# Kernel tuning notes

Hardware: AMD Instinct MI355X
Metric: run time of the kernel (lower is better)

Reference implementation:

```python
import jax, jax.numpy as jnp
import numpy as np
from jax import lax

E, C, H, W = 256, 128, 56, 56          # edges, stage-2 channels, spatial
NC, NP, NL, LL, FEAT = 200, 512, 64, 8, 64  # corners, corner-edge pairs, loops, loop len, loop feat
EDGE_DIM = 2 * C                        # 256 (image pooled + coord)
LOOP_IN = EDGE_DIM + 2                  # 258 (LoopEncoder input channels)


def _conv1d_relu(x, w, b):
    # x: [N, Cin, L]; ReflectionPad1d(1) + Conv1d(k=3) + ReLU
    x = jnp.pad(x, ((0, 0), (0, 0), (1, 1)), mode='reflect')
    y = lax.conv_general_dilated(x, w, (1,), 'VALID', dimension_numbers=('NCH', 'OIH', 'NCH'))
    return jax.nn.relu(y + b[None, :, None])


def setup_inputs() -> dict:
    key = jax.random.key(0)
    ks = jax.random.split(key, 16)
    p = lambda i, shape: jax.random.normal(ks[i], shape, jnp.float32) * 0.05
    return {
        'image_x': jax.random.normal(ks[0], (E, C, H, W), jnp.float32),
        'coord_x': jax.random.normal(ks[1], (E, C, 1, 1), jnp.float32),
        'corners': jax.random.uniform(ks[2], (NC, 2), jnp.float32),
        'corner_edge_pairs': jnp.stack([jax.random.randint(ks[3], (NP,), 0, NC),
                                        jax.random.randint(ks[4], (NP,), 0, E)], axis=1),
        'edge_corner': jax.random.randint(ks[5], (E, 2), 0, NC),
        'loops': jax.random.randint(ks[6], (NL, LL), 0, NC),
        'W_ep1': p(7, (64, EDGE_DIM)), 'b_ep1': jnp.zeros((64,), jnp.float32),
        'W_ep2': p(8, (1, 64)), 'b_ep2': jnp.zeros((1,), jnp.float32),
        'Wc0': p(9, (64, LOOP_IN, 3)), 'bc0': jnp.zeros((64,), jnp.float32),
        'Wc1': p(10, (64, 64, 3)), 'bc1': jnp.zeros((64,), jnp.float32),
        'Wc2': p(11, (64, 64, 3)), 'bc2': jnp.zeros((64,), jnp.float32),
        'Wl1': p(12, (32, 64)), 'bl1': jnp.zeros((32,), jnp.float32),
        'Wl2': p(13, (1, 32)), 'bl2': jnp.zeros((1,), jnp.float32),
        'W_agg': p(14, (C, C + FEAT)),
    }


def reference(image_x, coord_x, corners, corner_edge_pairs, edge_corner, loops,
              W_ep1, b_ep1, W_ep2, b_ep2, Wc0, bc0, Wc1, bc1, Wc2, bc2,
              Wl1, bl1, Wl2, bl2, W_agg):
    # edge features: global max-pool of per-edge image features + coord features
    edge_x = jnp.concatenate([image_x.max(axis=(-2, -1)), coord_x[:, :, 0, 0]], axis=1)  # [E, 2C]
    edge_conf = jax.nn.sigmoid(jax.nn.relu(edge_x @ W_ep1.T + b_ep1) @ W_ep2.T + b_ep2).ravel()  # [E]

    # scatter-mean edge features onto corners (index_add_ in torch)
    cf = jax.ops.segment_sum(edge_x[corner_edge_pairs[:, 1]], corner_edge_pairs[:, 0], num_segments=NC)
    cnt = jax.ops.segment_sum(jnp.ones((NP,), jnp.float32), corner_edge_pairs[:, 0], num_segments=NC)
    corner_features = cf / jnp.maximum(cnt, 1.0)[:, None]  # [NC, 2C]

    # LoopEncoder over each loop's corner sequence (vectorized over loops)
    loop_inp = jnp.concatenate([corner_features[loops], corners[loops]], axis=-1)  # [NL, LL, 2C+2]
    h = loop_inp.transpose(0, 2, 1)  # [NL, 2C+2, LL]
    h = _conv1d_relu(h, Wc0, bc0)
    h = _conv1d_relu(h, Wc1, bc1)
    h = _conv1d_relu(h, Wc2, bc2)
    loop_features = h.max(-1)  # [NL, 64]
    loop_conf = jax.nn.sigmoid(jax.nn.relu(loop_features @ Wl1.T + bl1) @ Wl2.T + bl2).ravel()  # [NL]

    # loop-edge incidence: edge (a,b) is in loop iff (a,b) appears as consecutive pair (either order)
    prev = jnp.roll(loops, 1, axis=1)
    nxt = jnp.roll(loops, -1, axis=1)
    pairs = jnp.concatenate([jnp.stack([loops, prev], -1), jnp.stack([loops, nxt], -1)], axis=1)  # [NL, 2LL, 2]
    loop_edges = (edge_corner[None, :, None, :] == pairs[:, None, :, :]).all(-1).any(-1)
    loop_edges = loop_edges.astype(jnp.float32)  # [NL, E]

    # confidence-weighted average of loop features per edge
    wgt = loop_conf[:, None, None] * loop_edges[..., None]  # [NL, E, 1]
    coord_features = (loop_features[:, None, :] * wgt).sum(0) / jnp.maximum(wgt.sum(0), 1e-4)  # [E, 64]

    # coord_aggregate: 1x1 conv (no bias) + ReLU
    out = jax.nn.relu(jnp.concatenate([coord_x[:, :, 0, 0], coord_features], axis=1) @ W_agg.T)  # [E, C]
    return out, edge_conf, loop_conf, loop_edges
```

## Files before the change

### kernel.cpp

```cpp
#include <hip/hip_runtime.h>
#include <math.h>

#define E_      256
#define C_      128
#define S_      3136
#define NC_     200
#define NP_     512
#define NL_     64
#define LL_     8
#define EDGE_DIM_ 256
#define LOOP_IN_  258
#define FEAT_   64

__global__ __launch_bounds__(256) void pool_kernel(const float* __restrict__ image_x,
                                                   float* __restrict__ edge_x) {
    int row  = blockIdx.x * 4 + (threadIdx.x >> 6);
    int lane = threadIdx.x & 63;
    const float4* p = reinterpret_cast<const float4*>(image_x) + (size_t)row * (S_ / 4);

    float m = -INFINITY;
    #pragma unroll
    for (int it = 0; it < 12; ++it) {
        float4 v = p[lane + it * 64];
        m = fmaxf(m, fmaxf(fmaxf(v.x, v.y), fmaxf(v.z, v.w)));
    }
    if (lane < 16) {
        float4 v = p[768 + lane];
        m = fmaxf(m, fmaxf(fmaxf(v.x, v.y), fmaxf(v.z, v.w)));
    }
    #pragma unroll
    for (int off = 32; off; off >>= 1) m = fmaxf(m, __shfl_down(m, off));
    if (lane == 0) {
        int e = row >> 7, c = row & 127;
        edge_x[e * EDGE_DIM_ + c] = m;
    }
}

__global__ void coord_copy_kernel(const float* __restrict__ coord_x,
                                  float* __restrict__ edge_x) {
    int i = blockIdx.x * 256 + threadIdx.x;
    int e = i >> 7, c = i & 127;
    edge_x[e * EDGE_DIM_ + C_ + c] = coord_x[i];
}

__global__ __launch_bounds__(64) void edge_conf_kernel(const float* __restrict__ edge_x,
                                                       const float* __restrict__ W1,
                                                       const float* __restrict__ b1,
                                                       const float* __restrict__ W2,
                                                       const float* __restrict__ b2,
                                                       float* __restrict__ out_conf) {
    int e = blockIdx.x, j = threadIdx.x;
    const float* x = edge_x + e * EDGE_DIM_;
    float acc = b1[j];
    for (int i = 0; i < EDGE_DIM_; ++i) acc += x[i] * W1[j * EDGE_DIM_ + i];
    float h = fmaxf(acc, 0.f) * W2[j];
    #pragma unroll
    for (int off = 32; off; off >>= 1) h += __shfl_down(h, off);
    if (j == 0) out_conf[e] = 1.f / (1.f + __expf(-(h + b2[0])));
}

__global__ __launch_bounds__(256) void corner_kernel(const float* __restrict__ edge_x,
                                                     const int* __restrict__ pairs,
                                                     float* __restrict__ corner_features) {
    __shared__ int sp[NP_ * 2];
    int corner = blockIdx.x;
    for (int i = threadIdx.x; i < NP_ * 2; i += 256) sp[i] = pairs[i];
    __syncthreads();
    int c = threadIdx.x;
    float sum = 0.f, cnt = 0.f;
    for (int p = 0; p < NP_; ++p) {
        if (sp[p * 2] == corner) { sum += edge_x[sp[p * 2 + 1] * EDGE_DIM_ + c]; cnt += 1.f; }
    }
    corner_features[corner * EDGE_DIM_ + c] = sum / fmaxf(cnt, 1.f);
}

__global__ __launch_bounds__(64) void loop_enc_kernel(
        const float* __restrict__ corner_features, const float* __restrict__ corners,
        const int* __restrict__ loops,
        const float* __restrict__ Wc0, const float* __restrict__ bc0,
        const float* __restrict__ Wc1, const float* __restrict__ bc1,
        const float* __restrict__ Wc2, const float* __restrict__ bc2,
        const float* __restrict__ Wl1, const float* __restrict__ bl1,
        const float* __restrict__ Wl2, const float* __restrict__ bl2,
        float* __restrict__ loop_features, float* __restrict__ out_loop_conf) {
    __shared__ float inp[LOOP_IN_][LL_];
    __shared__ float ha[64][LL_];
    __shared__ float hb[64][LL_];
    __shared__ float lf[64];
    __shared__ int cidx[LL_];

    int l = blockIdx.x, tid = threadIdx.x;
    if (tid < LL_) cidx[tid] = loops[l * LL_ + tid];
    __syncthreads();
    for (int idx = tid; idx < LOOP_IN_ * LL_; idx += 64) {
        int i = idx / LL_, j = idx % LL_;
        float v = (i < EDGE_DIM_) ? corner_features[cidx[j] * EDGE_DIM_ + i]
                                  : corners[cidx[j] * 2 + (i - EDGE_DIM_)];
        inp[i][j] = v;
    }
    __syncthreads();

    const int rm1[8] = {1, 0, 1, 2, 3, 4, 5, 6};
    const int rp1[8] = {1, 2, 3, 4, 5, 6, 7, 6};
    int o = tid;

    {
        float acc[LL_];
        float b = bc0[o];
        #pragma unroll
        for (int t = 0; t < LL_; ++t) acc[t] = b;
        for (int i = 0; i < LOOP_IN_; ++i) {
            float w0 = Wc0[(o * LOOP_IN_ + i) * 3 + 0];
            float w1 = Wc0[(o * LOOP_IN_ + i) * 3 + 1];
            float w2 = Wc0[(o * LOOP_IN_ + i) * 3 + 2];
            #pragma unroll
            for (int t = 0; t < LL_; ++t)
                acc[t] += w0 * inp[i][rm1[t]] + w1 * inp[i][t] + w2 * inp[i][rp1[t]];
        }
        #pragma unroll
        for (int t = 0; t < LL_; ++t) ha[o][t] = fmaxf(acc[t], 0.f);
    }
    __syncthreads();

    {
        float acc[LL_];
        float b = bc1[o];
        #pragma unroll
        for (int t = 0; t < LL_; ++t) acc[t] = b;
        for (int i = 0; i < 64; ++i) {
            float w0 = Wc1[(o * 64 + i) * 3 + 0];
            float w1 = Wc1[(o * 64 + i) * 3 + 1];
            float w2 = Wc1[(o * 64 + i) * 3 + 2];
            #pragma unroll
            for (int t = 0; t < LL_; ++t)
                acc[t] += w0 * ha[i][rm1[t]] + w1 * ha[i][t] + w2 * ha[i][rp1[t]];
        }
        #pragma unroll
        for (int t = 0; t < LL_; ++t) hb[o][t] = fmaxf(acc[t], 0.f);
    }
    __syncthreads();

    {
        float acc[LL_];
        float b = bc2[o];
        #pragma unroll
        for (int t = 0; t < LL_; ++t) acc[t] = b;
        for (int i = 0; i < 64; ++i) {
            float w0 = Wc2[(o * 64 + i) * 3 + 0];
            float w1 = Wc2[(o * 64 + i) * 3 + 1];
            float w2 = Wc2[(o * 64 + i) * 3 + 2];
            #pragma unroll
            for (int t = 0; t < LL_; ++t)
                acc[t] += w0 * hb[i][rm1[t]] + w1 * hb[i][t] + w2 * hb[i][rp1[t]];
        }
        float m = -INFINITY;
        #pragma unroll
        for (int t = 0; t < LL_; ++t) m = fmaxf(m, fmaxf(acc[t], 0.f));
        lf[o] = m;
        loop_features[l * FEAT_ + o] = m;
    }
    __syncthreads();

    float part = 0.f;
    if (tid < 32) {
        float a = bl1[tid];
        for (int o2 = 0; o2 < 64; ++o2) a += lf[o2] * Wl1[tid * 64 + o2];
        part = fmaxf(a, 0.f) * Wl2[tid];
    }
    #pragma unroll
    for (int off = 32; off; off >>= 1) part += __shfl_down(part, off);
    if (tid == 0) out_loop_conf[l] = 1.f / (1.f + __expf(-(part + bl2[0])));
}

__global__ __launch_bounds__(256) void loop_edges_kernel(const int* __restrict__ loops,
                                                         const int* __restrict__ edge_corner,
                                                         float* __restrict__ out_le) {
    __shared__ int lp[LL_];
    int l = blockIdx.x;
    if (threadIdx.x < LL_) lp[threadIdx.x] = loops[l * LL_ + threadIdx.x];
    __syncthreads();
    int e = threadIdx.x;
    int a = edge_corner[e * 2], b = edge_corner[e * 2 + 1];
    bool hit = false;
    #pragma unroll
    for (int j = 0; j < LL_; ++j) {
        int x = lp[j], pv = lp[(j + LL_ - 1) & 7], nx = lp[(j + 1) & 7];
        hit = hit || (a == x && (b == pv || b == nx));
    }
    out_le[l * E_ + e] = hit ? 1.f : 0.f;
}

__global__ __launch_bounds__(128) void final_kernel(const float* __restrict__ coord_x,
                                                    const float* __restrict__ loop_features,
                                                    const float* __restrict__ loop_conf,
                                                    const float* __restrict__ loop_edges,
                                                    const float* __restrict__ W_agg,
                                                    float* __restrict__ out) {
    __shared__ float cf[FEAT_];
    int e = blockIdx.x, tid = threadIdx.x;
    if (tid < FEAT_) {
        float num = 0.f, den = 0.f;
        for (int l = 0; l < NL_; ++l) {
            float w = loop_conf[l] * loop_edges[l * E_ + e];
            den += w;
            num += w * loop_features[l * FEAT_ + tid];
        }
        cf[tid] = num / fmaxf(den, 1e-4f);
    }
    __syncthreads();
    int c = tid;
    const float* wr = W_agg + c * (C_ + FEAT_);
    float acc = 0.f;
    for (int j = 0; j < C_; ++j) acc += coord_x[e * C_ + j] * wr[j];
    for (int f = 0; f < FEAT_; ++f) acc += cf[f] * wr[C_ + f];
    out[e * C_ + c] = fmaxf(acc, 0.f);
}

extern "C" void kernel_launch(void* const* d_in, const int* in_sizes, int n_in,
                              void* d_out, int out_size, void* d_ws, size_t ws_size,
                              hipStream_t stream) {
    const float* image_x     = (const float*)d_in[0];
    const float* coord_x     = (const float*)d_in[1];
    const float* corners     = (const float*)d_in[2];
    const int*   cep         = (const int*)d_in[3];
    const int*   edge_corner = (const int*)d_in[4];
    const int*   loops       = (const int*)d_in[5];
    const float* W_ep1 = (const float*)d_in[6];
    const float* b_ep1 = (const float*)d_in[7];
    const float* W_ep2 = (const float*)d_in[8];
    const float* b_ep2 = (const float*)d_in[9];
    const float* Wc0   = (const float*)d_in[10];
    const float* bc0   = (const float*)d_in[11];
    const float* Wc1   = (const float*)d_in[12];
    const float* bc1   = (const float*)d_in[13];
    const float* Wc2   = (const float*)d_in[14];
    const float* bc2   = (const float*)d_in[15];
    const float* Wl1   = (const float*)d_in[16];
    const float* bl1   = (const float*)d_in[17];
    const float* Wl2   = (const float*)d_in[18];
    const float* bl2   = (const float*)d_in[19];
    const float* W_agg = (const float*)d_in[20];

    float* out       = (float*)d_out;
    float* out_main  = out;
    float* out_econf = out + E_ * C_;
    float* out_lconf = out_econf + E_;
    float* out_le    = out_lconf + NL_;

    float* edge_x          = (float*)d_ws;
    float* corner_features = edge_x + E_ * EDGE_DIM_;
    float* loop_features   = corner_features + NC_ * EDGE_DIM_;

    pool_kernel<<<dim3(E_ * C_ / 4), dim3(256), 0, stream>>>(image_x, edge_x);
    coord_copy_kernel<<<dim3(E_ * C_ / 256), dim3(256), 0, stream>>>(coord_x, edge_x);
    edge_conf_kernel<<<dim3(E_), dim3(64), 0, stream>>>(edge_x, W_ep1, b_ep1, W_ep2, b_ep2, out_econf);
    corner_kernel<<<dim3(NC_), dim3(256), 0, stream>>>(edge_x, cep, corner_features);
    loop_enc_kernel<<<dim3(NL_), dim3(64), 0, stream>>>(corner_features, corners, loops,
                                                        Wc0, bc0, Wc1, bc1, Wc2, bc2,
                                                        Wl1, bl1, Wl2, bl2,
                                                        loop_features, out_lconf);
    loop_edges_kernel<<<dim3(NL_), dim3(256), 0, stream>>>(loops, edge_corner, out_le);
    final_kernel<<<dim3(E_), dim3(128), 0, stream>>>(coord_x, loop_features, out_lconf,
                                                     out_le, W_agg, out_main);
}
```

Measured before the change: 685.9 us.

## Fuse small kernels and split loop-encoder convolutions across four waves

Moves the coord copy into the pool kernel, and merges edge-confidence, corner averaging and loop-edge incidence into one kernel that branches on block index. This removes several launches and the gaps between them. The loop encoder now uses 256 threads, with each wave handling a quarter of the input channels and the partial sums reduced through shared memory. That adds parallelism to a 64-block kernel at the cost of extra syncs and shared-memory traffic. The pool kernel dominates runtime (about 411 MB read), so the gain is limited to launch overhead and the latency of the small serial stages.

```diff
diff --git a/kernel.cpp b/kernel.cpp
--- a/kernel.cpp
+++ b/kernel.cpp
@@ -13,6 +13,7 @@
 #define FEAT_   64
 
 __global__ __launch_bounds__(256) void pool_kernel(const float* __restrict__ image_x,
+                                                   const float* __restrict__ coord_x,
                                                    float* __restrict__ edge_x) {
     int row  = blockIdx.x * 4 + (threadIdx.x >> 6);
     int lane = threadIdx.x & 63;
@@ -33,48 +34,73 @@
     if (lane == 0) {
         int e = row >> 7, c = row & 127;
         edge_x[e * EDGE_DIM_ + c] = m;
-    }
-}
-
-__global__ void coord_copy_kernel(const float* __restrict__ coord_x,
-                                  float* __restrict__ edge_x) {
-    int i = blockIdx.x * 256 + threadIdx.x;
-    int e = i >> 7, c = i & 127;
-    edge_x[e * EDGE_DIM_ + C_ + c] = coord_x[i];
-}
-
-__global__ __launch_bounds__(64) void edge_conf_kernel(const float* __restrict__ edge_x,
-                                                       const float* __restrict__ W1,
-                                                       const float* __restrict__ b1,
-                                                       const float* __restrict__ W2,
-                                                       const float* __restrict__ b2,
-                                                       float* __restrict__ out_conf) {
-    int e = blockIdx.x, j = threadIdx.x;
-    const float* x = edge_x + e * EDGE_DIM_;
-    float acc = b1[j];
-    for (int i = 0; i < EDGE_DIM_; ++i) acc += x[i] * W1[j * EDGE_DIM_ + i];
-    float h = fmaxf(acc, 0.f) * W2[j];
-    #pragma unroll
-    for (int off = 32; off; off >>= 1) h += __shfl_down(h, off);
-    if (j == 0) out_conf[e] = 1.f / (1.f + __expf(-(h + b2[0])));
-}
-
-__global__ __launch_bounds__(256) void corner_kernel(const float* __restrict__ edge_x,
-                                                     const int* __restrict__ pairs,
-                                                     float* __restrict__ corner_features) {
-    __shared__ int sp[NP_ * 2];
-    int corner = blockIdx.x;
-    for (int i = threadIdx.x; i < NP_ * 2; i += 256) sp[i] = pairs[i];
-    __syncthreads();
-    int c = threadIdx.x;
-    float sum = 0.f, cnt = 0.f;
-    for (int p = 0; p < NP_; ++p) {
-        if (sp[p * 2] == corner) { sum += edge_x[sp[p * 2 + 1] * EDGE_DIM_ + c]; cnt += 1.f; }
-    }
-    corner_features[corner * EDGE_DIM_ + c] = sum / fmaxf(cnt, 1.f);
-}
-
-__global__ __launch_bounds__(64) void loop_enc_kernel(
+        edge_x[e * EDGE_DIM_ + C_ + c] = coord_x[row];
+    }
+}
+
+#define MID_A_  64
+#define MID_B_  (MID_A_ + NC_)
+#define MID_N_  (MID_B_ + NL_)
+
+__global__ __launch_bounds__(256) void mid_kernel(const float* __restrict__ edge_x,
+                                                  const float* __restrict__ W1,
+                                                  const float* __restrict__ b1,
+                                                  const float* __restrict__ W2,
+                                                  const float* __restrict__ b2,
+                                                  const int* __restrict__ pairs,
+                                                  const int* __restrict__ loops,
+                                                  const int* __restrict__ edge_corner,
+                                                  float* __restrict__ out_econf,
+                                                  float* __restrict__ corner_features,
+                                                  float* __restrict__ out_le) {
+    __shared__ float smem[4 * EDGE_DIM_];
+    int b = blockIdx.x, tid = threadIdx.x;
+
+    if (b < MID_A_) {
+        float* xs = smem;
+        for (int idx = tid; idx < 4 * EDGE_DIM_; idx += 256)
+            xs[idx] = edge_x[b * 4 * EDGE_DIM_ + idx];
+        __syncthreads();
+        int w = tid >> 6, j = tid & 63;
+        int e = b * 4 + w;
+        const float* x = xs + w * EDGE_DIM_;
+        const float* wr = W1 + j * EDGE_DIM_;
+        float acc = b1[j];
+        #pragma unroll 8
+        for (int i = 0; i < EDGE_DIM_; ++i) acc += x[i] * wr[i];
+        float h = fmaxf(acc, 0.f) * W2[j];
+        #pragma unroll
+        for (int off = 32; off; off >>= 1) h += __shfl_down(h, off);
+        if (j == 0) out_econf[e] = 1.f / (1.f + __expf(-(h + b2[0])));
+    } else if (b < MID_B_) {
+        int* sp = reinterpret_cast<int*>(smem);
+        int corner = b - MID_A_;
+        for (int i = tid; i < NP_ * 2; i += 256) sp[i] = pairs[i];
+        __syncthreads();
+        int c = tid;
+        float sum = 0.f, cnt = 0.f;
+        for (int p = 0; p < NP_; ++p) {
+            if (sp[p * 2] == corner) { sum += edge_x[sp[p * 2 + 1] * EDGE_DIM_ + c]; cnt += 1.f; }
+        }
+        corner_features[corner * EDGE_DIM_ + c] = sum / fmaxf(cnt, 1.f);
+    } else {
+        int* lp = reinterpret_cast<int*>(smem);
+        int l = b - MID_B_;
+        if (tid < LL_) lp[tid] = loops[l * LL_ + tid];
+        __syncthreads();
+        int e = tid;
+        int a = edge_corner[e * 2], bb = edge_corner[e * 2 + 1];
+        bool hit = false;
+        #pragma unroll
+        for (int j = 0; j < LL_; ++j) {
+            int x = lp[j], pv = lp[(j + LL_ - 1) & 7], nx = lp[(j + 1) & 7];
+            hit = hit || (a == x && (bb == pv || bb == nx));
+        }
+        out_le[l * E_ + e] = hit ? 1.f : 0.f;
+    }
+}
+
+__global__ __launch_bounds__(256) void loop_enc_kernel(
         const float* __restrict__ corner_features, const float* __restrict__ corners,
         const int* __restrict__ loops,
         const float* __restrict__ Wc0, const float* __restrict__ bc0,
@@ -83,111 +109,125 @@
         const float* __restrict__ Wl1, const float* __restrict__ bl1,
         const float* __restrict__ Wl2, const float* __restrict__ bl2,
         float* __restrict__ loop_features, float* __restrict__ out_loop_conf) {
-    __shared__ float inp[LOOP_IN_][LL_];
-    __shared__ float ha[64][LL_];
-    __shared__ float hb[64][LL_];
+    __shared__ float inp[LOOP_IN_ * LL_];
+    __shared__ float part[4 * 64 * 9];
+    __shared__ float ha[64 * 9];
+    __shared__ float hb[64 * 9];
     __shared__ float lf[64];
     __shared__ int cidx[LL_];
 
     int l = blockIdx.x, tid = threadIdx.x;
+    int o = tid & 63, s = tid >> 6;
     if (tid < LL_) cidx[tid] = loops[l * LL_ + tid];
     __syncthreads();
-    for (int idx = tid; idx < LOOP_IN_ * LL_; idx += 64) {
-        int i = idx / LL_, j = idx % LL_;
-        float v = (i < EDGE_DIM_) ? corner_features[cidx[j] * EDGE_DIM_ + i]
-                                  : corners[cidx[j] * 2 + (i - EDGE_DIM_)];
-        inp[i][j] = v;
+    for (int idx = tid; idx < LOOP_IN_ * LL_; idx += 256) {
+        int i = idx >> 3, j = idx & 7;
+        inp[idx] = (i < EDGE_DIM_) ? corner_features[cidx[j] * EDGE_DIM_ + i]
+                                   : corners[cidx[j] * 2 + (i - EDGE_DIM_)];
     }
     __syncthreads();
 
     const int rm1[8] = {1, 0, 1, 2, 3, 4, 5, 6};
     const int rp1[8] = {1, 2, 3, 4, 5, 6, 7, 6};
-    int o = tid;
 
     {
         float acc[LL_];
-        float b = bc0[o];
-        #pragma unroll
-        for (int t = 0; t < LL_; ++t) acc[t] = b;
-        for (int i = 0; i < LOOP_IN_; ++i) {
+        #pragma unroll
+        for (int t = 0; t < LL_; ++t) acc[t] = 0.f;
+        int lo = s * 64 + (s < 2 ? s : 2);
+        int hi = lo + (s < 2 ? 65 : 64);
+        for (int i = lo; i < hi; ++i) {
             float w0 = Wc0[(o * LOOP_IN_ + i) * 3 + 0];
             float w1 = Wc0[(o * LOOP_IN_ + i) * 3 + 1];
             float w2 = Wc0[(o * LOOP_IN_ + i) * 3 + 2];
+            const float* ip = inp + i * LL_;
             #pragma unroll
             for (int t = 0; t < LL_; ++t)
-                acc[t] += w0 * inp[i][rm1[t]] + w1 * inp[i][t] + w2 * inp[i][rp1[t]];
-        }
-        #pragma unroll
-        for (int t = 0; t < LL_; ++t) ha[o][t] = fmaxf(acc[t], 0.f);
+                acc[t] += w0 * ip[rm1[t]] + w1 * ip[t] + w2 * ip[rp1[t]];
+        }
+        #pragma unroll
+        for (int t = 0; t < LL_; ++t) part[(s * 64 + o) * 9 + t] = acc[t];
+    }
+    __syncthreads();
+    if (tid < 64) {
+        #pragma unroll
+        for (int t = 0; t < LL_; ++t) {
+            float v = bc0[tid];
+            #pragma unroll
+            for (int ss = 0; ss < 4; ++ss) v += part[(ss * 64 + tid) * 9 + t];
+            ha[tid * 9 + t] = fmaxf(v, 0.f);
+        }
     }
     __syncthreads();
 
     {
         float acc[LL_];
-        float b = bc1[o];
-        #pragma unroll
-        for (int t = 0; t < LL_; ++t) acc[t] = b;
-        for (int i = 0; i < 64; ++i) {
+        #pragma unroll
+        for (int t = 0; t < LL_; ++t) acc[t] = 0.f;
+        for (int i = s * 16; i < s * 16 + 16; ++i) {
             float w0 = Wc1[(o * 64 + i) * 3 + 0];
             float w1 = Wc1[(o * 64 + i) * 3 + 1];
             float w2 = Wc1[(o * 64 + i) * 3 + 2];
+            const float* ip = ha + i * 9;
             #pragma unroll
             for (int t = 0; t < LL_; ++t)
-                acc[t] += w0 * ha[i][rm1[t]] + w1 * ha[i][t] + w2 * ha[i][rp1[t]];
-        }
-        #pragma unroll
-        for (int t = 0; t < LL_; ++t) hb[o][t] = fmaxf(acc[t], 0.f);
+                acc[t] += w0 * ip[rm1[t]] + w1 * ip[t] + w2 * ip[rp1[t]];
+        }
+        #pragma unroll
+        for (int t = 0; t < LL_; ++t) part[(s * 64 + o) * 9 + t] = acc[t];
+    }
+    __syncthreads();
+    if (tid < 64) {
+        #pragma unroll
+        for (int t = 0; t < LL_; ++t) {
+            float v = bc1[tid];
+            #pragma unroll
+            for (int ss = 0; ss < 4; ++ss) v += part[(ss * 64 + tid) * 9 + t];
+            hb[tid * 9 + t] = fmaxf(v, 0.f);
+        }
     }
     __syncthreads();
 
     {
         float acc[LL_];
-        float b = bc2[o];
-        #pragma unroll
-        for (int t = 0; t < LL_; ++t) acc[t] = b;
-        for (int i = 0; i < 64; ++i) {
+        #pragma unroll
+        for (int t = 0; t < LL_; ++t) acc[t] = 0.f;
+        for (int i = s * 16; i < s * 16 + 16; ++i) {
             float w0 = Wc2[(o * 64 + i) * 3 + 0];
             float w1 = Wc2[(o * 64 + i) * 3 + 1];
             float w2 = Wc2[(o * 64 + i) * 3 + 2];
+            const float* ip = hb + i * 9;
             #pragma unroll
             for (int t = 0; t < LL_; ++t)
-                acc[t] += w0 * hb[i][rm1[t]] + w1 * hb[i][t] + w2 * hb[i][rp1[t]];
-        }
+                acc[t] += w0 * ip[rm1[t]] + w1 * ip[t] + w2 * ip[rp1[t]];
+        }
+        #pragma unroll
+        for (int t = 0; t < LL_; ++t) part[(s * 64 + o) * 9 + t] = acc[t];
+    }
+    __syncthreads();
+    if (tid < 64) {
         float m = -INFINITY;
         #pragma unroll
-        for (int t = 0; t < LL_; ++t) m = fmaxf(m, fmaxf(acc[t], 0.f));
-        lf[o] = m;
-        loop_features[l * FEAT_ + o] = m;
-    }
-    __syncthreads();
-
-    float part = 0.f;
+        for (int t = 0; t < LL_; ++t) {
+            float v = bc2[tid];
+            #pragma unroll
+            for (int ss = 0; ss < 4; ++ss) v += part[(ss * 64 + tid) * 9 + t];
+            m = fmaxf(m, fmaxf(v, 0.f));
+        }
+        lf[tid] = m;
+        loop_features[l * FEAT_ + tid] = m;
+    }
+    __syncthreads();
+
+    float pv = 0.f;
     if (tid < 32) {
         float a = bl1[tid];
         for (int o2 = 0; o2 < 64; ++o2) a += lf[o2] * Wl1[tid * 64 + o2];
-        part = fmaxf(a, 0.f) * Wl2[tid];
+        pv = fmaxf(a, 0.f) * Wl2[tid];
     }
     #pragma unroll
-    for (int off = 32; off; off >>= 1) part += __shfl_down(part, off);
-    if (tid == 0) out_loop_conf[l] = 1.f / (1.f + __expf(-(part + bl2[0])));
-}
-
-__global__ __launch_bounds__(256) void loop_edges_kernel(const int* __restrict__ loops,
-                                                         const int* __restrict__ edge_corner,
-                                                         float* __restrict__ out_le) {
-    __shared__ int lp[LL_];
-    int l = blockIdx.x;
-    if (threadIdx.x < LL_) lp[threadIdx.x] = loops[l * LL_ + threadIdx.x];
-    __syncthreads();
-    int e = threadIdx.x;
-    int a = edge_corner[e * 2], b = edge_corner[e * 2 + 1];
-    bool hit = false;
-    #pragma unroll
-    for (int j = 0; j < LL_; ++j) {
-        int x = lp[j], pv = lp[(j + LL_ - 1) & 7], nx = lp[(j + 1) & 7];
-        hit = hit || (a == x && (b == pv || b == nx));
-    }
-    out_le[l * E_ + e] = hit ? 1.f : 0.f;
+    for (int off = 32; off; off >>= 1) pv += __shfl_down(pv, off);
+    if (tid == 0) out_loop_conf[l] = 1.f / (1.f + __expf(-(pv + bl2[0])));
 }
 
 __global__ __launch_bounds__(128) void final_kernel(const float* __restrict__ coord_x,
@@ -251,15 +291,14 @@
     float* corner_features = edge_x + E_ * EDGE_DIM_;
     float* loop_features   = corner_features + NC_ * EDGE_DIM_;
 
-    pool_kernel<<<dim3(E_ * C_ / 4), dim3(256), 0, stream>>>(image_x, edge_x);
-    coord_copy_kernel<<<dim3(E_ * C_ / 256), dim3(256), 0, stream>>>(coord_x, edge_x);
-    edge_conf_kernel<<<dim3(E_), dim3(64), 0, stream>>>(edge_x, W_ep1, b_ep1, W_ep2, b_ep2, out_econf);
-    corner_kernel<<<dim3(NC_), dim3(256), 0, stream>>>(edge_x, cep, corner_features);
-    loop_enc_kernel<<<dim3(NL_), dim3(64), 0, stream>>>(corner_features, corners, loops,
-                                                        Wc0, bc0, Wc1, bc1, Wc2, bc2,
-                                                        Wl1, bl1, Wl2, bl2,
-                                                        loop_features, out_lconf);
-    loop_edges_kernel<<<dim3(NL_), dim3(256), 0, stream>>>(loops, edge_corner, out_le);
+    pool_kernel<<<dim3(E_ * C_ / 4), dim3(256), 0, stream>>>(image_x, coord_x, edge_x);
+    mid_kernel<<<dim3(MID_N_), dim3(256), 0, stream>>>(edge_x, W_ep1, b_ep1, W_ep2, b_ep2,
+                                                       cep, loops, edge_corner,
+                                                       out_econf, corner_features, out_le);
+    loop_enc_kernel<<<dim3(NL_), dim3(256), 0, stream>>>(corner_features, corners, loops,
+                                                         Wc0, bc0, Wc1, bc1, Wc2, bc2,
+                                                         Wl1, bl1, Wl2, bl2,
+                                                         loop_features, out_lconf);
     final_kernel<<<dim3(E_), dim3(128), 0, stream>>>(coord_x, loop_features, out_lconf,
                                                      out_le, W_agg, out_main);
 }
```

Measured after the change: 638.9 us. 6.9% less time.
